# Optimization experiments

Hardware: AMD Instinct MI355X
Metric: run time of the kernel (lower is better)

Reference implementation:

```python
import jax, jax.numpy as jnp
import numpy as np

N, D, H, E, TOP_K = 32768, 768, 256, 8, 2


def setup_inputs() -> dict:
    key = jax.random.key(0)
    ks = jax.random.split(key, 9)
    s_in = 1.0 / np.sqrt(D)
    s_hid = 1.0 / np.sqrt(H)
    return {
        "x": jax.random.normal(ks[0], (N, D), dtype=jnp.float32),
        # per-expert MLP weights, stacked over expert dim E
        "W1": jax.random.uniform(ks[1], (E, D, H), jnp.float32, -s_in, s_in),
        "b1": jax.random.uniform(ks[2], (E, H), jnp.float32, -s_in, s_in),
        "W2": jax.random.uniform(ks[3], (E, H, D), jnp.float32, -s_hid, s_hid),
        "b2": jax.random.uniform(ks[4], (E, D), jnp.float32, -s_hid, s_hid),
        # gate MLP: Linear(D,H) -> ReLU -> Linear(H,E)
        "Wg1": jax.random.uniform(ks[5], (D, H), jnp.float32, -s_in, s_in),
        "bg1": jax.random.uniform(ks[6], (H,), jnp.float32, -s_in, s_in),
        "Wg2": jax.random.uniform(ks[7], (H, E), jnp.float32, -s_hid, s_hid),
        "bg2": jax.random.uniform(ks[8], (E,), jnp.float32, -s_hid, s_hid),
    }


def reference(x, W1, b1, W2, b2, Wg1, bg1, Wg2, bg2):
    # gating
    gate_scores = jax.nn.relu(x @ Wg1 + bg1) @ Wg2 + bg2          # [N, E]
    gate_probs = jax.nn.softmax(gate_scores, axis=-1)              # [N, E]
    top_k_probs, top_k_idx = jax.lax.top_k(gate_probs, TOP_K)      # [N, K]
    top_k_probs = top_k_probs / jnp.sum(top_k_probs, axis=-1, keepdims=True)

    # dense all-expert compute (faithful to original: every expert on every token)
    h = jax.nn.relu(jnp.einsum("nd,edh->enh", x, W1) + b1[:, None, :])  # [E, N, H]
    expert_out = jnp.einsum("enh,ehd->end", h, W2) + b2[:, None, :]      # [E, N, D]

    # gather selected experts per token and combine
    tok = jnp.arange(x.shape[0])[:, None]                          # [N, 1]
    sel = expert_out[top_k_idx, tok, :]                            # [N, K, D]
    output = jnp.sum(top_k_probs[..., None] * sel, axis=1)          # [N, D]
    return output, gate_probs
```

## Files before the change

kernel.cpp:

```cpp
#include <hip/hip_runtime.h>
#include <hip/hip_bf16.h>
#include <stdint.h>

#define NTOK 32768
#define DIM  768
#define HID  256
#define NEXP 8
#define PADC 144

typedef float f32x4 __attribute__((ext_vector_type(4)));
typedef short s16x8 __attribute__((ext_vector_type(8)));

__device__ __forceinline__ unsigned short f2bf(float f) {
  union { float f; unsigned int u; } c; c.f = f;
  unsigned int r = c.u + 0x7fffu + ((c.u >> 16) & 1u);
  return (unsigned short)(r >> 16);
}

__device__ __forceinline__ float bf2f(unsigned int u) {
  union { unsigned int x; float f; } c; c.x = u << 16; return c.f;
}

__device__ __forceinline__ unsigned short f2h(float f) {
  union { _Float16 h; unsigned short u; } c; c.h = (_Float16)f; return c.u;
}

__device__ __forceinline__ float h2f(unsigned short u) {
  union { unsigned short u; _Float16 h; } c; c.u = u; return (float)c.h;
}

__device__ __forceinline__ void gload_lds16(const unsigned short* g, unsigned short* l) {
  __builtin_amdgcn_global_load_lds((const __attribute__((address_space(1))) void*)g,
                                   (__attribute__((address_space(3))) void*)l, 16, 0, 0);
}

__global__ __launch_bounds__(256) void k_cvt_x(const float* __restrict__ x,
                                               unsigned short* __restrict__ xf16) {
  int i = (blockIdx.x * 256 + threadIdx.x) * 8;
  float4 a = *(const float4*)(x + i);
  float4 b = *(const float4*)(x + i + 4);
  float f[8] = {a.x, a.y, a.z, a.w, b.x, b.y, b.z, b.w};
  unsigned short hh[8];
#pragma unroll
  for (int q = 0; q < 8; ++q) hh[q] = f2h(f[q]);
  int4 vh;
  vh.x = (int)((unsigned)hh[0] | ((unsigned)hh[1] << 16));
  vh.y = (int)((unsigned)hh[2] | ((unsigned)hh[3] << 16));
  vh.z = (int)((unsigned)hh[4] | ((unsigned)hh[5] << 16));
  vh.w = (int)((unsigned)hh[6] | ((unsigned)hh[7] << 16));
  *(int4*)(xf16 + i) = vh;
}

__global__ __launch_bounds__(256) void k_trh(const float* __restrict__ in,
                                             unsigned short* __restrict__ outp,
                                             int R, int C) {
  __shared__ float tile[32][33];
  int e = blockIdx.z;
  const float* ip = in + (size_t)e * R * C;
  unsigned short* op = outp + (size_t)e * R * C;
  int tx = threadIdx.x & 31, ty = threadIdx.x >> 5;
  int r0 = blockIdx.y * 32, c0 = blockIdx.x * 32;
#pragma unroll
  for (int i = 0; i < 4; ++i)
    tile[ty + i * 8][tx] = ip[(size_t)(r0 + ty + i * 8) * C + c0 + tx];
  __syncthreads();
#pragma unroll
  for (int i = 0; i < 4; ++i)
    op[(size_t)(c0 + ty + i * 8) * R + r0 + tx] = f2h(tile[tx][ty + i * 8]);
}

__global__ __launch_bounds__(256) void k_gmfma(const unsigned short* __restrict__ xh,
                                               const unsigned short* __restrict__ wh,
                                               const float* __restrict__ bg1,
                                               unsigned short* __restrict__ hg) {
  int bm = blockIdx.x * 128;
  int bn = blockIdx.y * 128;

  __shared__ __align__(16) unsigned short Ah[128 * 64];
  __shared__ __align__(16) unsigned short Bh[128 * 64];

  int tid = threadIdx.x;
  int lane = tid & 63;
  int wid = tid >> 6;
  int wm = wid >> 1, wn = wid & 1;
  int ar = lane & 15, kg = lane >> 4;

  const unsigned short *sah[4], *sbh[4];
  unsigned short *dA[4], *dB[4];
#pragma unroll
  for (int i = 0; i < 4; ++i) {
    int cb0 = i * 256 + wid * 64;
    int ci = cb0 + lane;
    int row = ci >> 3;
    int cb = (ci & 7) ^ (row & 7);
    sah[i] = xh + (size_t)(bm + row) * DIM + cb * 8;
    sbh[i] = wh + (size_t)(bn + row) * DIM + cb * 8;
    dA[i] = &Ah[cb0 * 8];
    dB[i] = &Bh[cb0 * 8];
  }

  f32x4 acc[4][4] = {};

  for (int kt = 0; kt < DIM / 64; ++kt) {
#pragma unroll
    for (int i = 0; i < 4; ++i) {
      gload_lds16(sah[i] + kt * 64, dA[i]);
      gload_lds16(sbh[i] + kt * 64, dB[i]);
    }
    __syncthreads();
#pragma unroll
    for (int ks = 0; ks < 2; ++ks) {
      int kc = ks * 4 + kg;
      s16x8 a[4], b[4];
#pragma unroll
      for (int m = 0; m < 4; ++m) {
        int row = wm * 64 + m * 16 + ar;
        a[m] = *(const s16x8*)&Ah[row * 64 + ((kc ^ (row & 7)) * 8)];
      }
#pragma unroll
      for (int n = 0; n < 4; ++n) {
        int row = wn * 64 + n * 16 + ar;
        b[n] = *(const s16x8*)&Bh[row * 64 + ((kc ^ (row & 7)) * 8)];
      }
#pragma unroll
      for (int m = 0; m < 4; ++m)
#pragma unroll
        for (int n = 0; n < 4; ++n)
          acc[m][n] = __builtin_amdgcn_mfma_f32_16x16x32_f16(a[m], b[n], acc[m][n], 0, 0, 0);
    }
    __syncthreads();
  }

#pragma unroll
  for (int n = 0; n < 4; ++n) {
    int col = bn + wn * 64 + n * 16 + ar;
    float bb = bg1[col];
#pragma unroll
    for (int m = 0; m < 4; ++m) {
      int rbase = bm + wm * 64 + m * 16 + kg * 4;
#pragma unroll
      for (int r = 0; r < 4; ++r)
        hg[(size_t)(rbase + r) * HID + col] = f2h(fmaxf(acc[m][n][r] + bb, 0.f));
    }
  }
}

__global__ __launch_bounds__(256) void k_gate2a(const unsigned short* __restrict__ hg,
                                                const float* __restrict__ wg2,
                                                const float* __restrict__ bg2,
                                                float* __restrict__ gs,
                                                int* __restrict__ rcnt,
                                                int* __restrict__ rlist) {
  int tok = blockIdx.x * 256 + threadIdx.x;
  const unsigned short* hrow = hg + (size_t)tok * HID;

  float s[8];
#pragma unroll
  for (int e = 0; e < 8; ++e) s[e] = bg2[e];
#pragma unroll 4
  for (int j = 0; j < 32; ++j) {
    s16x8 hv8 = *(const s16x8*)(hrow + j * 8);
#pragma unroll
    for (int i = 0; i < 8; ++i) {
      float hv = h2f((unsigned short)hv8[i]);
      const float* wr = wg2 + (j * 8 + i) * 8;
#pragma unroll
      for (int e = 0; e < 8; ++e) s[e] += hv * wr[e];
    }
  }

  f32x4 o0 = {s[0], s[1], s[2], s[3]};
  f32x4 o1 = {s[4], s[5], s[6], s[7]};
  *(f32x4*)&gs[(size_t)tok * 8] = o0;
  *(f32x4*)&gs[(size_t)tok * 8 + 4] = o1;

  float m1 = -3e38f, m2 = -3e38f, m3 = -3e38f;
#pragma unroll
  for (int e = 0; e < 8; ++e) {
    float v = s[e];
    if (v > m1)      { m3 = m2; m2 = m1; m1 = v; }
    else if (v > m2) { m3 = m2; m2 = v; }
    else if (v > m3) { m3 = v; }
  }
  if (m2 - m3 < 1e-3f) {
    int i = atomicAdd(rcnt, 1);
    rlist[i] = tok;
  }
}

__global__ __launch_bounds__(256) void k_rescue(const float* __restrict__ x,
                                                const float* __restrict__ wg1,
                                                const float* __restrict__ bg1,
                                                const float* __restrict__ wg2,
                                                const float* __restrict__ bg2,
                                                const int* __restrict__ rcnt,
                                                const int* __restrict__ rlist,
                                                float* __restrict__ gs) {
  __shared__ float xs[DIM];
  __shared__ float ps[4][8];
  int n = rcnt[0];
  int tid = threadIdx.x;
  int lane = tid & 63, wid = tid >> 6;
  for (int idx = blockIdx.x; idx < n; idx += 2048) {
    int tok = rlist[idx];
    __syncthreads();
#pragma unroll
    for (int q = 0; q < 3; ++q) xs[tid + q * 256] = x[(size_t)tok * DIM + tid + q * 256];
    __syncthreads();
    const float* wcol = wg1 + tid;
    float pa[8] = {};
#pragma unroll 4
    for (int k0 = 0; k0 < DIM; k0 += 8) {
#pragma unroll
      for (int q = 0; q < 8; ++q)
        pa[q] = fmaf(xs[k0 + q], wcol[(size_t)(k0 + q) * HID], pa[q]);
    }
    float acc = bg1[tid] +
                (((pa[0] + pa[1]) + (pa[2] + pa[3])) + ((pa[4] + pa[5]) + (pa[6] + pa[7])));
    float hj = fmaxf(acc, 0.f);
    float p[8];
#pragma unroll
    for (int e = 0; e < 8; ++e) p[e] = hj * wg2[tid * 8 + e];
#pragma unroll
    for (int off = 32; off >= 1; off >>= 1) {
#pragma unroll
      for (int e = 0; e < 8; ++e) p[e] += __shfl_xor(p[e], off);
    }
    if (lane == 0) {
#pragma unroll
      for (int e = 0; e < 8; ++e) ps[wid][e] = p[e];
    }
    __syncthreads();
    if (tid < 8)
      gs[(size_t)tok * 8 + tid] = bg2[tid] + ps[0][tid] + ps[1][tid] + ps[2][tid] + ps[3][tid];
  }
}

__global__ __launch_bounds__(256) void k_gate2b(const float* __restrict__ gs,
                                                float* __restrict__ gprob,
                                                int* __restrict__ cnt,
                                                int* __restrict__ lists,
                                                float* __restrict__ wts) {
  __shared__ int lcnt[8];
  __shared__ int sbase[8];
  __shared__ int se1[256], se2[256], sp1[256], sp2[256];
  __shared__ float sw1[256], sw2[256];
  int tid = threadIdx.x;
  if (tid < 8) lcnt[tid] = 0;
  __syncthreads();

  int tok = blockIdx.x * 256 + tid;
  f32x4 s0v = *(const f32x4*)&gs[(size_t)tok * 8];
  f32x4 s1v = *(const f32x4*)&gs[(size_t)tok * 8 + 4];
  float s[8] = {s0v[0], s0v[1], s0v[2], s0v[3], s1v[0], s1v[1], s1v[2], s1v[3]};

  float m = s[0];
#pragma unroll
  for (int e = 1; e < 8; ++e) m = fmaxf(m, s[e]);
  float p[8]; float sum = 0.f;
#pragma unroll
  for (int e = 0; e < 8; ++e) { p[e] = expf(s[e] - m); sum += p[e]; }
  float inv = 1.f / sum;
#pragma unroll
  for (int e = 0; e < 8; ++e) p[e] *= inv;

  f32x4 o0 = {p[0], p[1], p[2], p[3]};
  f32x4 o1 = {p[4], p[5], p[6], p[7]};
  *(f32x4*)&gprob[(size_t)tok * 8] = o0;
  *(f32x4*)&gprob[(size_t)tok * 8 + 4] = o1;

  int e1 = 0; float p1 = p[0];
#pragma unroll
  for (int e = 1; e < 8; ++e) if (p[e] > p1) { p1 = p[e]; e1 = e; }
  int e2 = -1; float p2 = -1.f;
#pragma unroll
  for (int e = 0; e < 8; ++e) if (e != e1 && p[e] > p2) { p2 = p[e]; e2 = e; }
  float rinv = 1.f / (p1 + p2);

  int pos1 = atomicAdd(&lcnt[e1], 1);
  int pos2 = atomicAdd(&lcnt[e2], 1);
  se1[tid] = e1; sp1[tid] = pos1; sw1[tid] = p1 * rinv;
  se2[tid] = e2; sp2[tid] = pos2; sw2[tid] = p2 * rinv;
  __syncthreads();

  if (tid < 8) sbase[tid] = atomicAdd(&cnt[tid * 32], lcnt[tid]);
  __syncthreads();

  int a1i = sbase[se1[tid]] + sp1[tid];
  lists[se1[tid] * NTOK + a1i] = tok; wts[se1[tid] * NTOK + a1i] = sw1[tid];
  int a2i = sbase[se2[tid]] + sp2[tid];
  lists[se2[tid] * NTOK + a2i] = tok; wts[se2[tid] * NTOK + a2i] = -sw2[tid];
}

__global__ __launch_bounds__(256) void k_ffn1(const unsigned short* __restrict__ xf16,
                                              const unsigned short* __restrict__ w1t,
                                              const float* __restrict__ b1,
                                              const int* __restrict__ cnt,
                                              const int* __restrict__ lists,
                                              unsigned short* __restrict__ h) {
  int id = blockIdx.x;
  int xcd = id & 7, local = id >> 3;
  int bny = local & 1;
  int r2 = local >> 1;
  int xh = r2 & 31, e = r2 >> 5;
  int row0 = ((xh << 3) | xcd) * 128;
  int bn = bny * 128;

  int c = cnt[e * 32];
  if (row0 >= c) return;
  int pfx = 0;
#pragma unroll
  for (int j = 0; j < 8; ++j) if (j < e) pfx += cnt[j * 32];

  __shared__ __align__(16) unsigned short smem[128 * PADC];
  __shared__ int stok[128];
  unsigned short* As = smem;
  unsigned short* Bs = smem + 128 * 64;

  int tid = threadIdx.x;
  int lane = tid & 63;
  int wid = tid >> 6;
  int wm = wid >> 1, wn = wid & 1;
  int ar = lane & 15, kg = lane >> 4;

  if (tid < 128) stok[tid] = lists[e * NTOK + min(row0 + tid, c - 1)];
  __syncthreads();

  const unsigned short* asrc[4];
  const unsigned short* bsrc[4];
  unsigned short* ldsA[4];
  unsigned short* ldsB[4];
#pragma unroll
  for (int i = 0; i < 4; ++i) {
    int cb0 = i * 256 + wid * 64;
    int ci = cb0 + lane;
    int row = ci >> 3;
    int cb = (ci & 7) ^ (row & 7);
    asrc[i] = xf16 + (size_t)stok[row] * DIM + cb * 8;
    bsrc[i] = w1t + ((size_t)e * HID + bn + row) * DIM + cb * 8;
    ldsA[i] = &As[cb0 * 8];
    ldsB[i] = &Bs[cb0 * 8];
  }

  f32x4 acc[4][4] = {};

  for (int kt = 0; kt < DIM / 64; ++kt) {
#pragma unroll
    for (int i = 0; i < 4; ++i) {
      gload_lds16(asrc[i] + kt * 64, ldsA[i]);
      gload_lds16(bsrc[i] + kt * 64, ldsB[i]);
    }
    __syncthreads();
#pragma unroll
    for (int ks = 0; ks < 2; ++ks) {
      int kc = ks * 4 + kg;
      s16x8 a[4], b[4];
#pragma unroll
      for (int m = 0; m < 4; ++m) {
        int row = wm * 64 + m * 16 + ar;
        a[m] = *(const s16x8*)&As[row * 64 + ((kc ^ (row & 7)) * 8)];
      }
#pragma unroll
      for (int n = 0; n < 4; ++n) {
        int row = wn * 64 + n * 16 + ar;
        b[n] = *(const s16x8*)&Bs[row * 64 + ((kc ^ (row & 7)) * 8)];
      }
#pragma unroll
      for (int m = 0; m < 4; ++m)
#pragma unroll
        for (int n = 0; n < 4; ++n)
          acc[m][n] = __builtin_amdgcn_mfma_f32_16x16x32_f16(a[m], b[n], acc[m][n], 0, 0, 0);
    }
    __syncthreads();
  }

#pragma unroll
  for (int n = 0; n < 4; ++n) {
    int col = wn * 64 + n * 16 + ar;
    float bb = b1[e * HID + bn + col];
#pragma unroll
    for (int m = 0; m < 4; ++m) {
      int rloc = wm * 64 + m * 16 + kg * 4;
#pragma unroll
      for (int r = 0; r < 4; ++r)
        smem[(rloc + r) * PADC + col] = f2h(fmaxf(acc[m][n][r] + bb, 0.f));
    }
  }
  __syncthreads();
  int hbase = pfx + row0;
#pragma unroll
  for (int q = 0; q < 8; ++q) {
    int ci = tid + q * 256;
    int row = ci >> 4, ch = ci & 15;
    if (row0 + row < c) {
      int4 v = *(const int4*)&smem[row * PADC + ch * 8];
      *(int4*)&h[(size_t)(hbase + row) * HID + bn + ch * 8] = v;
    }
  }
}

template <bool STORE_PART>
__global__ __launch_bounds__(256) void k_ffn2(const unsigned short* __restrict__ h,
                                              const unsigned short* __restrict__ w2t,
                                              const float* __restrict__ b2,
                                              const int* __restrict__ cnt,
                                              const int* __restrict__ lists,
                                              const float* __restrict__ wts,
                                              unsigned short* __restrict__ part0,
                                              unsigned short* __restrict__ part1,
                                              float* __restrict__ out) {
  int id = blockIdx.x;
  int xcd = id & 7, local = id >> 3;
  int bny = local % 6;
  int r2 = local / 6;
  int xh = r2 & 31, e = r2 >> 5;
  int row0 = ((xh << 3) | xcd) * 128;
  int bn = bny * 128;

  int c = cnt[e * 32];
  if (row0 >= c) return;
  int pfx = 0;
#pragma unroll
  for (int j = 0; j < 8; ++j) if (j < e) pfx += cnt[j * 32];

  __shared__ __align__(16) unsigned short smem[128 * PADC];
  __shared__ int stok[128];
  __shared__ float swt[128];
  unsigned short* As = smem;
  unsigned short* Bs = smem + 128 * 64;

  int tid = threadIdx.x;
  int lane = tid & 63;
  int wid = tid >> 6;
  int wm = wid >> 1, wn = wid & 1;
  int ar = lane & 15, kg = lane >> 4;

  if (tid < 128) {
    int r = row0 + tid;
    stok[tid] = (r < c) ? lists[e * NTOK + r] : 0;
    swt[tid]  = (r < c) ? wts[e * NTOK + r] : 0.f;
  }
  __syncthreads();

  const unsigned short* asrc[4];
  const unsigned short* bsrc[4];
  unsigned short* ldsA[4];
  unsigned short* ldsB[4];
#pragma unroll
  for (int i = 0; i < 4; ++i) {
    int cb0 = i * 256 + wid * 64;
    int ci = cb0 + lane;
    int row = ci >> 3;
    int cb = (ci & 7) ^ (row & 7);
    asrc[i] = h + (size_t)(pfx + row0 + row) * HID + cb * 8;
    bsrc[i] = w2t + ((size_t)e * DIM + bn + row) * HID + cb * 8;
    ldsA[i] = &As[cb0 * 8];
    ldsB[i] = &Bs[cb0 * 8];
  }

  f32x4 acc[4][4] = {};

  for (int kt = 0; kt < HID / 64; ++kt) {
#pragma unroll
    for (int i = 0; i < 4; ++i) {
      gload_lds16(asrc[i] + kt * 64, ldsA[i]);
      gload_lds16(bsrc[i] + kt * 64, ldsB[i]);
    }
    __syncthreads();
#pragma unroll
    for (int ks = 0; ks < 2; ++ks) {
      int kc = ks * 4 + kg;
      s16x8 a[4], b[4];
#pragma unroll
      for (int m = 0; m < 4; ++m) {
        int row = wm * 64 + m * 16 + ar;
        a[m] = *(const s16x8*)&As[row * 64 + ((kc ^ (row & 7)) * 8)];
      }
#pragma unroll
      for (int n = 0; n < 4; ++n) {
        int row = wn * 64 + n * 16 + ar;
        b[n] = *(const s16x8*)&Bs[row * 64 + ((kc ^ (row & 7)) * 8)];
      }
#pragma unroll
      for (int m = 0; m < 4; ++m)
#pragma unroll
        for (int n = 0; n < 4; ++n)
          acc[m][n] = __builtin_amdgcn_mfma_f32_16x16x32_f16(a[m], b[n], acc[m][n], 0, 0, 0);
    }
    __syncthreads();
  }

  if constexpr (STORE_PART) {
#pragma unroll
    for (int n = 0; n < 4; ++n) {
      int col = wn * 64 + n * 16 + ar;
      float bb = b2[e * DIM + bn + col];
#pragma unroll
      for (int m = 0; m < 4; ++m) {
        int rloc = wm * 64 + m * 16 + kg * 4;
#pragma unroll
        for (int r = 0; r < 4; ++r) {
          float w = swt[rloc + r];
          smem[(rloc + r) * PADC + col] = f2bf((acc[m][n][r] + bb) * fabsf(w));
        }
      }
    }
    __syncthreads();
#pragma unroll
    for (int q = 0; q < 8; ++q) {
      int ci = tid + q * 256;
      int row = ci >> 4, ch = ci & 15;
      float w = swt[row];
      if (w != 0.f) {
        unsigned short* dst = (w > 0.f) ? part0 : part1;
        int4 v = *(const int4*)&smem[row * PADC + ch * 8];
        *(int4*)&dst[(size_t)stok[row] * DIM + bn + ch * 8] = v;
      }
    }
  } else {
#pragma unroll
    for (int n = 0; n < 4; ++n) {
      int col = bn + wn * 64 + n * 16 + ar;
      float bb = b2[e * DIM + col];
#pragma unroll
      for (int m = 0; m < 4; ++m) {
        int rloc = wm * 64 + m * 16 + kg * 4;
#pragma unroll
        for (int r = 0; r < 4; ++r) {
          float w = swt[rloc + r];
          if (w != 0.f) {
            float v = (acc[m][n][r] + bb) * fabsf(w);
            atomicAdd(&out[(size_t)stok[rloc + r] * DIM + col], v);
          }
        }
      }
    }
  }
}

__global__ __launch_bounds__(256) void k_combine(const unsigned short* __restrict__ p0,
                                                 const unsigned short* __restrict__ p1,
                                                 float* __restrict__ out) {
  size_t i = ((size_t)blockIdx.x * 256 + threadIdx.x) * 8;
  int4 a = *(const int4*)(p0 + i);
  int4 b = *(const int4*)(p1 + i);
  unsigned int ua[4] = {(unsigned)a.x, (unsigned)a.y, (unsigned)a.z, (unsigned)a.w};
  unsigned int ub[4] = {(unsigned)b.x, (unsigned)b.y, (unsigned)b.z, (unsigned)b.w};
  float o[8];
#pragma unroll
  for (int q = 0; q < 4; ++q) {
    o[q * 2 + 0] = bf2f(ua[q] & 0xffffu) + bf2f(ub[q] & 0xffffu);
    o[q * 2 + 1] = bf2f(ua[q] >> 16)     + bf2f(ub[q] >> 16);
  }
  *(float4*)(out + i)     = *(float4*)&o[0];
  *(float4*)(out + i + 4) = *(float4*)&o[4];
}

extern "C" void kernel_launch(void* const* d_in, const int* in_sizes, int n_in,
                              void* d_out, int out_size, void* d_ws, size_t ws_size,
                              hipStream_t stream) {
  const float* x   = (const float*)d_in[0];
  const float* W1  = (const float*)d_in[1];
  const float* b1  = (const float*)d_in[2];
  const float* W2  = (const float*)d_in[3];
  const float* b2  = (const float*)d_in[4];
  const float* Wg1 = (const float*)d_in[5];
  const float* bg1 = (const float*)d_in[6];
  const float* Wg2 = (const float*)d_in[7];
  const float* bg2 = (const float*)d_in[8];
  float* out = (float*)d_out;
  float* gprob = out + (size_t)NTOK * DIM;

  char* ws = (char*)d_ws;
  size_t off = 0;
  auto alloc = [&](size_t bytes) { void* pp = ws + off; off += (bytes + 255) & ~(size_t)255; return pp; };
  unsigned short* w1t = (unsigned short*)alloc((size_t)NEXP * HID * DIM * 2);
  unsigned short* w2t = (unsigned short*)alloc((size_t)NEXP * DIM * HID * 2);
  float* hgbuf = (float*)alloc((size_t)NTOK * HID * 4);
  int* cnt = (int*)alloc(NEXP * 32 * 4);
  int* lists = (int*)alloc((size_t)NEXP * NTOK * 4);
  float* wts = (float*)alloc((size_t)NEXP * NTOK * 4);
  unsigned short* part0 = (unsigned short*)alloc((size_t)NTOK * DIM * 2);
  unsigned short* part1 = (unsigned short*)alloc((size_t)NTOK * DIM * 2);
  bool store_mode = (off <= ws_size);

  unsigned short *xf16, *wg1t;
  float* gs; int* rcnt; int* rlist;
  if (store_mode) {
    xf16 = part1;
    wg1t = part0;
    char* p0b = (char*)part0;
    gs    = (float*)(p0b + (1u << 20));
    rcnt  = (int*)(p0b + 9 * (1u << 18));
    rlist = (int*)(p0b + 10 * (1u << 18));
  } else {
    xf16  = (unsigned short*)alloc((size_t)NTOK * DIM * 2);
    wg1t  = (unsigned short*)alloc((size_t)DIM * HID * 2);
    gs    = (float*)alloc((size_t)NTOK * 8 * 4);
    rcnt  = (int*)alloc(256);
    rlist = (int*)alloc((size_t)NTOK * 4);
  }

  unsigned short* hg = (unsigned short*)hgbuf;
  unsigned short* h = (unsigned short*)hgbuf;

  hipMemsetAsync(cnt, 0, NEXP * 32 * sizeof(int), stream);
  hipMemsetAsync(rcnt, 0, sizeof(int), stream);
  if (!store_mode)
    hipMemsetAsync(d_out, 0, (size_t)NTOK * DIM * sizeof(float), stream);

  k_cvt_x<<<(NTOK * DIM) / (256 * 8), 256, 0, stream>>>(x, xf16);
  k_trh<<<dim3(HID / 32, DIM / 32, 1), 256, 0, stream>>>(Wg1, wg1t, DIM, HID);
  k_trh<<<dim3(HID / 32, DIM / 32, NEXP), 256, 0, stream>>>(W1, w1t, DIM, HID);
  k_trh<<<dim3(DIM / 32, HID / 32, NEXP), 256, 0, stream>>>(W2, w2t, HID, DIM);
  k_gmfma<<<dim3(NTOK / 128, HID / 128), 256, 0, stream>>>(xf16, wg1t, bg1, hg);
  k_gate2a<<<NTOK / 256, 256, 0, stream>>>(hg, Wg2, bg2, gs, rcnt, rlist);
  k_rescue<<<2048, 256, 0, stream>>>(x, Wg1, bg1, Wg2, bg2, rcnt, rlist, gs);
  k_gate2b<<<NTOK / 256, 256, 0, stream>>>(gs, gprob, cnt, lists, wts);
  k_ffn1<<<(NTOK / 128) * 2 * NEXP, 256, 0, stream>>>(xf16, w1t, b1, cnt, lists, h);
  if (store_mode) {
    k_ffn2<true><<<(NTOK / 128) * 6 * NEXP, 256, 0, stream>>>(h, w2t, b2, cnt, lists, wts, part0, part1, out);
    k_combine<<<(NTOK * DIM) / (256 * 8), 256, 0, stream>>>(part0, part1, out);
  } else {
    k_ffn2<false><<<(NTOK / 128) * 6 * NEXP, 256, 0, stream>>>(h, w2t, b2, cnt, lists, wts, part0, part1, out);
  }
}
```

Measured before the change: 247.3 us.

## Widen FFN1 tile to full hidden width with 512-thread blocks

Each FFN1 block now covers all 256 hidden columns for its 128 gathered tokens using 8 waves, where before two blocks each covered 128 columns. The gathered x rows are therefore loaded from global memory once instead of twice, which cuts A-side gather traffic. The epilogue writes out in two halves through shared memory with extra barriers. The block uses more LDS and threads, which may reduce occupancy and leaves half as many blocks to spread across CUs.

```diff
diff --git a/kernel.cpp b/kernel.cpp
--- a/kernel.cpp
+++ b/kernel.cpp
@@ -292,7 +292,7 @@
   lists[se2[tid] * NTOK + a2i] = tok; wts[se2[tid] * NTOK + a2i] = -sw2[tid];
 }
 
-__global__ __launch_bounds__(256) void k_ffn1(const unsigned short* __restrict__ xf16,
+__global__ __launch_bounds__(512) void k_ffn1(const unsigned short* __restrict__ xf16,
                                               const unsigned short* __restrict__ w1t,
                                               const float* __restrict__ b1,
                                               const int* __restrict__ cnt,
@@ -300,11 +300,8 @@
                                               unsigned short* __restrict__ h) {
   int id = blockIdx.x;
   int xcd = id & 7, local = id >> 3;
-  int bny = local & 1;
-  int r2 = local >> 1;
-  int xh = r2 & 31, e = r2 >> 5;
+  int xh = local & 31, e = local >> 5;
   int row0 = ((xh << 3) | xcd) * 128;
-  int bn = bny * 128;
 
   int c = cnt[e * 32];
   if (row0 >= c) return;
@@ -312,44 +309,48 @@
 #pragma unroll
   for (int j = 0; j < 8; ++j) if (j < e) pfx += cnt[j * 32];
 
-  __shared__ __align__(16) unsigned short smem[128 * PADC];
+  __shared__ __align__(16) unsigned short smem[(1024 + 2048) * 8];
   __shared__ int stok[128];
-  unsigned short* As = smem;
-  unsigned short* Bs = smem + 128 * 64;
 
   int tid = threadIdx.x;
   int lane = tid & 63;
   int wid = tid >> 6;
-  int wm = wid >> 1, wn = wid & 1;
+  int wm = wid >> 2, wn = wid & 3;
   int ar = lane & 15, kg = lane >> 4;
 
   if (tid < 128) stok[tid] = lists[e * NTOK + min(row0 + tid, c - 1)];
   __syncthreads();
 
-  const unsigned short* asrc[4];
-  const unsigned short* bsrc[4];
-  unsigned short* ldsA[4];
-  unsigned short* ldsB[4];
-#pragma unroll
-  for (int i = 0; i < 4; ++i) {
-    int cb0 = i * 256 + wid * 64;
+  const unsigned short* asrc[2];
+  unsigned short* ldsA[2];
+#pragma unroll
+  for (int q = 0; q < 2; ++q) {
+    int cb0 = q * 512 + wid * 64;
     int ci = cb0 + lane;
     int row = ci >> 3;
     int cb = (ci & 7) ^ (row & 7);
-    asrc[i] = xf16 + (size_t)stok[row] * DIM + cb * 8;
-    bsrc[i] = w1t + ((size_t)e * HID + bn + row) * DIM + cb * 8;
-    ldsA[i] = &As[cb0 * 8];
-    ldsB[i] = &Bs[cb0 * 8];
+    asrc[q] = xf16 + (size_t)stok[row] * DIM + cb * 8;
+    ldsA[q] = &smem[cb0 * 8];
+  }
+  const unsigned short* bsrc[4];
+  unsigned short* ldsB[4];
+#pragma unroll
+  for (int q = 0; q < 4; ++q) {
+    int cb0 = q * 512 + wid * 64;
+    int ci = cb0 + lane;
+    int row = ci >> 3;
+    int cb = (ci & 7) ^ (row & 7);
+    bsrc[q] = w1t + ((size_t)e * HID + row) * DIM + cb * 8;
+    ldsB[q] = &smem[8192 + cb0 * 8];
   }
 
   f32x4 acc[4][4] = {};
 
   for (int kt = 0; kt < DIM / 64; ++kt) {
 #pragma unroll
-    for (int i = 0; i < 4; ++i) {
-      gload_lds16(asrc[i] + kt * 64, ldsA[i]);
-      gload_lds16(bsrc[i] + kt * 64, ldsB[i]);
-    }
+    for (int q = 0; q < 2; ++q) gload_lds16(asrc[q] + kt * 64, ldsA[q]);
+#pragma unroll
+    for (int q = 0; q < 4; ++q) gload_lds16(bsrc[q] + kt * 64, ldsB[q]);
     __syncthreads();
 #pragma unroll
     for (int ks = 0; ks < 2; ++ks) {
@@ -358,12 +359,12 @@
 #pragma unroll
       for (int m = 0; m < 4; ++m) {
         int row = wm * 64 + m * 16 + ar;
-        a[m] = *(const s16x8*)&As[row * 64 + ((kc ^ (row & 7)) * 8)];
+        a[m] = *(const s16x8*)&smem[row * 64 + ((kc ^ (row & 7)) * 8)];
       }
 #pragma unroll
       for (int n = 0; n < 4; ++n) {
         int row = wn * 64 + n * 16 + ar;
-        b[n] = *(const s16x8*)&Bs[row * 64 + ((kc ^ (row & 7)) * 8)];
+        b[n] = *(const s16x8*)&smem[8192 + row * 64 + ((kc ^ (row & 7)) * 8)];
       }
 #pragma unroll
       for (int m = 0; m < 4; ++m)
@@ -374,28 +375,34 @@
     __syncthreads();
   }
 
-#pragma unroll
-  for (int n = 0; n < 4; ++n) {
-    int col = wn * 64 + n * 16 + ar;
-    float bb = b1[e * HID + bn + col];
-#pragma unroll
-    for (int m = 0; m < 4; ++m) {
-      int rloc = wm * 64 + m * 16 + kg * 4;
-#pragma unroll
-      for (int r = 0; r < 4; ++r)
-        smem[(rloc + r) * PADC + col] = f2h(fmaxf(acc[m][n][r] + bb, 0.f));
-    }
-  }
-  __syncthreads();
   int hbase = pfx + row0;
-#pragma unroll
-  for (int q = 0; q < 8; ++q) {
-    int ci = tid + q * 256;
-    int row = ci >> 4, ch = ci & 15;
-    if (row0 + row < c) {
-      int4 v = *(const int4*)&smem[row * PADC + ch * 8];
-      *(int4*)&h[(size_t)(hbase + row) * HID + bn + ch * 8] = v;
-    }
+#pragma unroll 1
+  for (int half = 0; half < 2; ++half) {
+    if ((wn >> 1) == half) {
+#pragma unroll
+      for (int n = 0; n < 4; ++n) {
+        int col = (wn & 1) * 64 + n * 16 + ar;
+        float bb = b1[e * HID + half * 128 + col];
+#pragma unroll
+        for (int m = 0; m < 4; ++m) {
+          int rloc = wm * 64 + m * 16 + kg * 4;
+#pragma unroll
+          for (int r = 0; r < 4; ++r)
+            smem[(rloc + r) * PADC + col] = f2h(fmaxf(acc[m][n][r] + bb, 0.f));
+        }
+      }
+    }
+    __syncthreads();
+#pragma unroll
+    for (int q = 0; q < 4; ++q) {
+      int ci = tid + q * 512;
+      int row = ci >> 4, ch = ci & 15;
+      if (row0 + row < c) {
+        int4 v = *(const int4*)&smem[row * PADC + ch * 8];
+        *(int4*)&h[(size_t)(hbase + row) * HID + half * 128 + ch * 8] = v;
+      }
+    }
+    __syncthreads();
   }
 }
 
@@ -617,7 +624,7 @@
   k_gate2a<<<NTOK / 256, 256, 0, stream>>>(hg, Wg2, bg2, gs, rcnt, rlist);
   k_rescue<<<2048, 256, 0, stream>>>(x, Wg1, bg1, Wg2, bg2, rcnt, rlist, gs);
   k_gate2b<<<NTOK / 256, 256, 0, stream>>>(gs, gprob, cnt, lists, wts);
-  k_ffn1<<<(NTOK / 128) * 2 * NEXP, 256, 0, stream>>>(xf16, w1t, b1, cnt, lists, h);
+  k_ffn1<<<(NTOK / 128) * NEXP, 512, 0, stream>>>(xf16, w1t, b1, cnt, lists, h);
   if (store_mode) {
     k_ffn2<true><<<(NTOK / 128) * 6 * NEXP, 256, 0, stream>>>(h, w2t, b2, cnt, lists, wts, part0, part1, out);
     k_combine<<<(NTOK * DIM) / (256 * 8), 256, 0, stream>>>(part0, part1, out);
```

Measured after the change: 240.7 us. 2.7% less time.
